# Kernel tuning notes

Hardware: AMD Instinct MI355X
Metric: run time of the kernel (lower is better)

## Reference

```python
import jax, jax.numpy as jnp
import numpy as np

N, C, H, W = 32, 512, 32, 32
K = 64  # num_clusters
D_OUT = 256


def _l2n(v, axis):
    # torch F.normalize: v / max(||v||, 1e-12)
    n = jnp.linalg.norm(v, axis=axis, keepdims=True)
    return v / jnp.maximum(n, 1e-12)


def _bn(v, gamma, beta):
    # BatchNorm1d, training mode (batch stats, biased variance), eps=1e-5
    m = v.mean(axis=0)
    var = ((v - m) ** 2).mean(axis=0)
    return (v - m) / jnp.sqrt(var + 1e-5) * gamma + beta


def setup_inputs() -> dict:
    key = jax.random.key(0)
    ks = jax.random.split(key, 5)
    x = jax.random.normal(ks[0], (N, C, H, W), dtype=jnp.float32)
    conv_w = jax.random.normal(ks[1], (K, C), dtype=jnp.float32) * 0.05
    centroids = jax.random.uniform(ks[2], (K, C), dtype=jnp.float32)
    hidden_w = jax.random.normal(ks[3], (K * C, D_OUT), dtype=jnp.float32) / jnp.sqrt(jnp.float32(C))
    gating_w = jax.random.normal(ks[4], (D_OUT, D_OUT), dtype=jnp.float32) / jnp.sqrt(jnp.float32(D_OUT))
    return {
        "x": x,
        "conv_w": conv_w,
        "centroids": centroids,
        "hidden_w": hidden_w,
        "bn2_gamma": jnp.ones((D_OUT,), jnp.float32),
        "bn2_beta": jnp.zeros((D_OUT,), jnp.float32),
        "gating_w": gating_w,
        "gbn_gamma": jnp.ones((D_OUT,), jnp.float32),
        "gbn_beta": jnp.zeros((D_OUT,), jnp.float32),
    }


def reference(x, conv_w, centroids, hidden_w, bn2_gamma, bn2_beta, gating_w, gbn_gamma, gbn_beta):
    n = x.shape[0]
    # descriptor-wise L2 normalization over channel dim
    x = _l2n(x, axis=1)                                  # [N,C,H,W]
    xf = x.reshape(n, x.shape[1], -1)                    # [N,C,S]
    # 1x1 conv -> soft assignment, softmax over clusters
    sa = jnp.einsum('ncs,kc->nks', xf, conv_w)           # [N,K,S]
    sa = jax.nn.softmax(sa, axis=1)
    # matmul-form NetVLAD: sum_s a[n,k,s]*(x[n,c,s]-cent[k,c])
    vlad = jnp.einsum('nks,ncs->nkc', sa, xf) \
         - sa.sum(axis=-1)[..., None] * centroids[None]  # [N,K,C]
    vlad = _l2n(vlad, axis=2)                            # intra-normalization
    vlad = _l2n(vlad.reshape(n, -1), axis=1)             # [N,K*C]
    v = vlad @ hidden_w                                  # [N,256]
    v = _bn(v, bn2_gamma, bn2_beta)
    # context gating
    gates = jax.nn.sigmoid(_bn(v @ gating_w, gbn_gamma, gbn_beta))
    return v * gates
```

## Files before the change

kernel.cpp:

```cpp
#include <hip/hip_runtime.h>
#include <math.h>

static constexpr int Nb = 32;
static constexpr int Cc = 512;
static constexpr int Ss = 1024;
static constexpr int Kk = 64;
static constexpr int Dd = 256;

typedef __attribute__((ext_vector_type(8))) short bf16x8;
typedef __attribute__((ext_vector_type(4))) float f32x4;
typedef __attribute__((ext_vector_type(4))) unsigned int u32x4;

union FragU { u32x4 u; bf16x8 h; };

__device__ __forceinline__ unsigned hi_pack(float x0, float x1) {
    return __builtin_amdgcn_perm(__float_as_uint(x1), __float_as_uint(x0), 0x07060302u);
}
__device__ __forceinline__ float trunc_hi(float x) {
    return __uint_as_float(__float_as_uint(x) & 0xFFFF0000u);
}
__device__ __forceinline__ void split8(const float* xv, FragU& bh, FragU& bl) {
#pragma unroll
    for (int p = 0; p < 4; ++p) {
        bh.u[p] = hi_pack(xv[2*p], xv[2*p+1]);
        float l0 = xv[2*p]   - trunc_hi(xv[2*p]);
        float l1 = xv[2*p+1] - trunc_hi(xv[2*p+1]);
        bl.u[p] = hi_pack(l0, l1);
    }
}

__device__ __forceinline__ void gload_lds16(const void* g, void* l) {
    __builtin_amdgcn_global_load_lds(
        (const __attribute__((address_space(1))) void*)g,
        (__attribute__((address_space(3))) void*)l, 16, 0, 0);
}

__global__ __launch_bounds__(256) void kprep_cw(
    const float* __restrict__ cw, short* __restrict__ cwh, short* __restrict__ cwl)
{
    int t = blockIdx.x * 256 + threadIdx.x;
    float4 v = *(const float4*)&cw[4 * (size_t)t];
    unsigned h0 = hi_pack(v.x, v.y), h1 = hi_pack(v.z, v.w);
    float l0 = v.x - trunc_hi(v.x), l1 = v.y - trunc_hi(v.y);
    float l2 = v.z - trunc_hi(v.z), l3 = v.w - trunc_hi(v.w);
    unsigned g0 = hi_pack(l0, l1), g1 = hi_pack(l2, l3);
    ((uint2*)cwh)[t] = make_uint2(h0, h1);
    ((uint2*)cwl)[t] = make_uint2(g0, g1);
}

__global__ __launch_bounds__(512) void k1_sa(
    const float* __restrict__ x, const short* __restrict__ cw_hi,
    const short* __restrict__ cw_lo, short* __restrict__ a_hi,
    short* __restrict__ a_lo, float* __restrict__ asum_part)
{
    __shared__ float xt[3 * 2048];
    __shared__ short cwh_t[3 * 4096];
    __shared__ short cwl_t[3 * 4096];
    __shared__ float redm[4][32];
    __shared__ float reds[4][32];

    const int tid = threadIdx.x;
    const int w = tid >> 6, lane = tid & 63;
    const int m = w & 3, sg = w >> 2;
    const int l15 = lane & 15, lg = lane >> 4;
    const int n = blockIdx.y, s0 = blockIdx.x * 32;

    const int strow = lane >> 3;
    const int stchk = lane & 7;
    const int xrow = 8 * w + strow;
    const int krow = 8 * w + strow;
    const int cwchk = stchk ^ (krow & 7);

    const float* xsrc = x + (size_t)n * Cc * Ss + s0 + 4 * stchk;

    auto GL = [&](int t) {
        const int b = t % 3;
        gload_lds16(xsrc + (size_t)(t * 64 + xrow) * Ss,
                    (char*)xt + b * 8192 + w * 1024);
        gload_lds16(cw_hi + (size_t)krow * Cc + t * 64 + cwchk * 8,
                    (char*)cwh_t + b * 8192 + w * 1024);
        gload_lds16(cw_lo + (size_t)krow * Cc + t * 64 + cwchk * 8,
                    (char*)cwl_t + b * 8192 + w * 1024);
    };

    f32x4 acc = {0.f, 0.f, 0.f, 0.f};
    float ssq = 0.f;
    const int sl = 16 * sg + l15;

    GL(0);
    GL(1);

    for (int ct = 0; ct < 8; ++ct) {
        if (ct < 7) { asm volatile("s_waitcnt vmcnt(3)" ::: "memory"); }
        else        { asm volatile("s_waitcnt vmcnt(0)" ::: "memory"); }
        __builtin_amdgcn_sched_barrier(0);
        __builtin_amdgcn_s_barrier();
        __builtin_amdgcn_sched_barrier(0);

        const int b = ct % 3;
#pragma unroll
        for (int ks = 0; ks < 2; ++ks) {
            const int cb = 32 * ks + 8 * lg;
            float xv[8];
#pragma unroll
            for (int j = 0; j < 8; ++j) xv[j] = xt[b * 2048 + (cb + j) * 32 + sl];
#pragma unroll
            for (int j = 0; j < 8; ++j) ssq += xv[j] * xv[j];
            FragU bh, bl;
            split8(xv, bh, bl);
            FragU ah, al;
            const int cslot = ((4 * ks + lg) ^ (l15 & 7)) * 8;
            ah.u = *(const u32x4*)&cwh_t[b * 4096 + (16 * m + l15) * 64 + cslot];
            al.u = *(const u32x4*)&cwl_t[b * 4096 + (16 * m + l15) * 64 + cslot];
            acc = __builtin_amdgcn_mfma_f32_16x16x32_bf16(al.h, bh.h, acc, 0, 0, 0);
            acc = __builtin_amdgcn_mfma_f32_16x16x32_bf16(ah.h, bl.h, acc, 0, 0, 0);
            acc = __builtin_amdgcn_mfma_f32_16x16x32_bf16(ah.h, bh.h, acc, 0, 0, 0);
        }
        if (ct < 6) GL(ct + 2);
    }

    ssq += __shfl_xor(ssq, 16);
    ssq += __shfl_xor(ssq, 32);
    const float inv = 1.f / fmaxf(sqrtf(ssq), 1e-12f);

    float sv[4];
    float mmax = -1e30f;
#pragma unroll
    for (int r = 0; r < 4; ++r) {
        sv[r] = acc[r] * inv;
        mmax = fmaxf(mmax, sv[r]);
    }
    mmax = fmaxf(mmax, __shfl_xor(mmax, 16));
    mmax = fmaxf(mmax, __shfl_xor(mmax, 32));
    if (lg == 0) redm[m][sl] = mmax;
    __syncthreads();
    mmax = fmaxf(fmaxf(redm[0][sl], redm[1][sl]),
                 fmaxf(redm[2][sl], redm[3][sl]));
    float den = 0.f;
#pragma unroll
    for (int r = 0; r < 4; ++r) {
        sv[r] = expf(sv[r] - mmax);
        den += sv[r];
    }
    den += __shfl_xor(den, 16);
    den += __shfl_xor(den, 32);
    if (lg == 0) reds[m][sl] = den;
    __syncthreads();
    den = reds[0][sl] + reds[1][sl] + reds[2][sl] + reds[3][sl];
    const float rinv = 1.f / den;

    const int scol = s0 + sl;
#pragma unroll
    for (int r = 0; r < 4; ++r) {
        const float a = sv[r] * rinv;
        const int k = 16 * m + 4 * lg + r;
        float t = a;
        t += __shfl_xor(t, 1); t += __shfl_xor(t, 2);
        t += __shfl_xor(t, 4); t += __shfl_xor(t, 8);
        if (l15 == 0)
            asum_part[((size_t)(n * Kk + k) << 6) + blockIdx.x * 2 + sg] = t;
        const float av = a * inv;
        const unsigned u = __float_as_uint(av);
        const float hv = __uint_as_float(u & 0xFFFF0000u);
        const size_t idx = (size_t)(n * Kk + k) * Ss + scol;
        a_hi[idx] = (short)(u >> 16);
        a_lo[idx] = (short)(__float_as_uint(av - hv) >> 16);
    }
}

__global__ __launch_bounds__(256) void kasum(
    const float* __restrict__ asum_part, float* __restrict__ asum)
{
    int row = blockIdx.x * 256 + threadIdx.x;
    const float* p = &asum_part[(size_t)row << 6];
    float s = 0.f;
#pragma unroll
    for (int i = 0; i < 16; ++i) {
        float4 v = *(const float4*)&p[4 * i];
        s += v.x + v.y + v.z + v.w;
    }
    asum[row] = s;
}

__global__ __launch_bounds__(512) void k2_vlad(
    const float* __restrict__ x, const short* __restrict__ a_hi,
    const short* __restrict__ a_lo, const float* __restrict__ centroids,
    const float* __restrict__ asum, float* __restrict__ vp0,
    float* __restrict__ vp1)
{
    __shared__ float xt[3 * 2048];
    __shared__ float asum_l[64];

    const int tid = threadIdx.x;
    const int w = tid >> 6, lane = tid & 63;
    const int wq = w & 3, wh = w >> 2;
    const int l15 = lane & 15, lg = lane >> 4;
    const int n = blockIdx.x, cp = blockIdx.y, sh = blockIdx.z;

    if (sh == 1 && tid < 64) asum_l[tid] = asum[n * Kk + tid];

    const int strow = lane >> 3;
    const int xrow = 8 * w + strow;
    const int stchk = (lane & 7) ^ (xrow & 7);
    const float* xsrc = x + (size_t)(n * Cc + cp * 64 + xrow) * Ss
                      + sh * 512 + 4 * stchk;

    auto GLx = [&](int t) {
        gload_lds16(xsrc + t * 32, (char*)xt + (t % 3) * 8192 + w * 1024);
    };

    const short* ahb = a_hi + (size_t)n * Kk * Ss + sh * 512;
    const short* alb = a_lo + (size_t)n * Kk * Ss + sh * 512;
    const int m0 = 2 * wh, m1 = 2 * wh + 1;
    const size_t arow0 = (size_t)(16 * m0 + l15) * Ss;
    const size_t arow1 = (size_t)(16 * m1 + l15) * Ss;

    f32x4 zero4 = {0.f, 0.f, 0.f, 0.f};
    f32x4 acc0 = zero4, acc1 = zero4;

    FragU ah0c, al0c, ah1c, al1c;
    FragU ah0n, al0n, ah1n, al1n;

    GLx(0);
    GLx(1);
    {
        const int so = 8 * lg;
        ah0c.u = *(const u32x4*)&ahb[arow0 + so];
        al0c.u = *(const u32x4*)&alb[arow0 + so];
        ah1c.u = *(const u32x4*)&ahb[arow1 + so];
        al1c.u = *(const u32x4*)&alb[arow1 + so];
    }

    for (int t = 0; t < 16; ++t) {
        if (t < 15) { asm volatile("s_waitcnt vmcnt(5)" ::: "memory"); }
        else        { asm volatile("s_waitcnt vmcnt(4)" ::: "memory"); }
        __builtin_amdgcn_sched_barrier(0);
        __builtin_amdgcn_s_barrier();
        __builtin_amdgcn_sched_barrier(0);

        if (t < 15) {
            const int so = (t + 1) * 32 + 8 * lg;
            ah0n.u = *(const u32x4*)&ahb[arow0 + so];
            al0n.u = *(const u32x4*)&alb[arow0 + so];
            ah1n.u = *(const u32x4*)&ahb[arow1 + so];
            al1n.u = *(const u32x4*)&alb[arow1 + so];
        }

        const int b = t % 3;
        const int cl = 16 * wq + l15;
        const int q0 = (2 * lg)     ^ (l15 & 7);
        const int q1 = (2 * lg + 1) ^ (l15 & 7);
        float4 xq0 = *(const float4*)&xt[b * 2048 + cl * 32 + q0 * 4];
        float4 xq1 = *(const float4*)&xt[b * 2048 + cl * 32 + q1 * 4];
        float xv[8] = {xq0.x, xq0.y, xq0.z, xq0.w, xq1.x, xq1.y, xq1.z, xq1.w};
        FragU bh, bl;
        split8(xv, bh, bl);

        acc0 = __builtin_amdgcn_mfma_f32_16x16x32_bf16(al0c.h, bh.h, acc0, 0, 0, 0);
        acc0 = __builtin_amdgcn_mfma_f32_16x16x32_bf16(ah0c.h, bl.h, acc0, 0, 0, 0);
        acc0 = __builtin_amdgcn_mfma_f32_16x16x32_bf16(ah0c.h, bh.h, acc0, 0, 0, 0);
        acc1 = __builtin_amdgcn_mfma_f32_16x16x32_bf16(al1c.h, bh.h, acc1, 0, 0, 0);
        acc1 = __builtin_amdgcn_mfma_f32_16x16x32_bf16(ah1c.h, bl.h, acc1, 0, 0, 0);
        acc1 = __builtin_amdgcn_mfma_f32_16x16x32_bf16(ah1c.h, bh.h, acc1, 0, 0, 0);

        ah0c.u = ah0n.u; al0c.u = al0n.u;
        ah1c.u = ah1n.u; al1c.u = al1n.u;

        if (t < 14) GLx(t + 2);
    }

    float* dst = sh ? vp1 : vp0;
    const int c = cp * 64 + 16 * wq + l15;
#pragma unroll
    for (int mi = 0; mi < 2; ++mi) {
        const f32x4 a4 = mi ? acc1 : acc0;
        const int m = 2 * wh + mi;
#pragma unroll
        for (int r = 0; r < 4; ++r) {
            const int k = 16 * m + 4 * lg + r;
            float val = a4[r];
            if (sh == 1) val -= asum_l[k] * centroids[(size_t)k * Cc + c];
            dst[(size_t)(n * Kk + k) * Cc + c] = val;
        }
    }
}

__global__ __launch_bounds__(512) void k3a_norm(
    float* __restrict__ vlad, const float* __restrict__ vp1,
    float* __restrict__ nrm)
{
    const int tid = threadIdx.x;
    const int w = tid >> 6, lane = tid & 63;
    const int n = blockIdx.x, kg = blockIdx.y;
    const int row = (n * Kk) + kg * 8 + w;
    const size_t base = (size_t)row * Cc + lane * 8;

    float4 v0 = *(const float4*)&vlad[base];
    float4 v1 = *(const float4*)&vlad[base + 4];
    float4 u0 = *(const float4*)&vp1[base];
    float4 u1 = *(const float4*)&vp1[base + 4];
    v0.x += u0.x; v0.y += u0.y; v0.z += u0.z; v0.w += u0.w;
    v1.x += u1.x; v1.y += u1.y; v1.z += u1.z; v1.w += u1.w;
    *(float4*)&vlad[base] = v0;
    *(float4*)&vlad[base + 4] = v1;
    float ssq = v0.x*v0.x + v0.y*v0.y + v0.z*v0.z + v0.w*v0.w
              + v1.x*v1.x + v1.y*v1.y + v1.z*v1.z + v1.w*v1.w;
#pragma unroll
    for (int off = 32; off >= 1; off >>= 1) ssq += __shfl_xor(ssq, off);
    if (lane == 0) nrm[row] = sqrtf(ssq);
}

__global__ __launch_bounds__(64) void k3b_scale(
    const float* __restrict__ nrm, float* __restrict__ scale)
{
    const int n = blockIdx.x, k = threadIdx.x;
    float r = nrm[n * Kk + k];
    float rn = r / fmaxf(r, 1e-12f);
    float p = rn * rn;
#pragma unroll
    for (int off = 32; off >= 1; off >>= 1) p += __shfl_xor(p, off);
    float g = sqrtf(p);
    scale[n * Kk + k] = 1.f / (fmaxf(r, 1e-12f) * fmaxf(g, 1e-12f));
}

__global__ __launch_bounds__(512) void k4_hidden(
    const float* __restrict__ vlad, const float* __restrict__ scale,
    const float* __restrict__ hw, float* __restrict__ vpart)
{
    __shared__ float vl[128][33];
    __shared__ float scale_l[32];
    const int tid = threadIdx.x;
    const int kc0 = blockIdx.x * 128;
    const int k = kc0 >> 9;
    if (tid < 32) scale_l[tid] = scale[tid * Kk + k];
    __syncthreads();
#pragma unroll
    for (int i = 0; i < 8; ++i) {
        int idx = tid + i * 512;
        int nn = idx >> 7, kcl = idx & 127;
        vl[kcl][nn] = vlad[(size_t)nn * (Kk * Cc) + kc0 + kcl] * scale_l[nn];
    }
    __syncthreads();

    const int d4 = tid & 63, ng = tid >> 6;
    float4 acc4[4];
#pragma unroll
    for (int j = 0; j < 4; ++j) acc4[j] = make_float4(0.f, 0.f, 0.f, 0.f);

    for (int kcl = 0; kcl < 128; ++kcl) {
        const float4 wv = *(const float4*)&hw[(size_t)(kc0 + kcl) * Dd + d4 * 4];
#pragma unroll
        for (int j = 0; j < 4; ++j) {
            float vn = vl[kcl][4 * ng + j];
            acc4[j].x += vn * wv.x; acc4[j].y += vn * wv.y;
            acc4[j].z += vn * wv.z; acc4[j].w += vn * wv.w;
        }
    }
#pragma unroll
    for (int j = 0; j < 4; ++j)
        *(float4*)&vpart[((size_t)blockIdx.x * Nb + 4 * ng + j) * Dd + d4 * 4] = acc4[j];
}

__global__ __launch_bounds__(128) void k5a_reduce(
    const float* __restrict__ vpart, float* __restrict__ v)
{
    int flat = blockIdx.x * 128 + threadIdx.x;
    float s = 0.f;
#pragma unroll 8
    for (int ch = 0; ch < 256; ++ch) s += vpart[(size_t)ch * (Nb * Dd) + flat];
    v[flat] = s;
}

__global__ __launch_bounds__(256) void k5bc_gate(
    const float* __restrict__ v, const float* __restrict__ gamma,
    const float* __restrict__ beta, const float* __restrict__ gw,
    float* __restrict__ v_bn, float* __restrict__ g_raw)
{
    __shared__ float vb[Dd];
    const int n = blockIdx.x, d = threadIdx.x;

    float s1 = 0.f;
#pragma unroll 8
    for (int i = 0; i < Nb; ++i) s1 += v[i * Dd + d];
    float mean = s1 * (1.f / Nb);
    float var = 0.f;
#pragma unroll 8
    for (int i = 0; i < Nb; ++i) {
        float t = v[i * Dd + d] - mean;
        var += t * t;
    }
    var *= (1.f / Nb);
    float inv = rsqrtf(var + 1e-5f);
    float vbn = (v[n * Dd + d] - mean) * inv * gamma[d] + beta[d];
    vb[d] = vbn;
    v_bn[n * Dd + d] = vbn;
    __syncthreads();

    float acc = 0.f;
#pragma unroll 8
    for (int c = 0; c < Dd; ++c) acc += vb[c] * gw[c * Dd + d];
    g_raw[n * Dd + d] = acc;
}

__global__ __launch_bounds__(256) void k5d_out(
    const float* __restrict__ g_raw, const float* __restrict__ v_bn,
    const float* __restrict__ ggamma, const float* __restrict__ gbeta,
    float* __restrict__ out)
{
    const int d = threadIdx.x;
    float vals[Nb];
    float s1 = 0.f;
#pragma unroll
    for (int n = 0; n < Nb; ++n) {
        vals[n] = g_raw[n * Dd + d];
        s1 += vals[n];
    }
    float m = s1 * (1.f / Nb);
    float var = 0.f;
#pragma unroll
    for (int n = 0; n < Nb; ++n) {
        float t = vals[n] - m;
        var += t * t;
    }
    var *= (1.f / Nb);
    float inv = rsqrtf(var + 1e-5f);
    float g = ggamma[d], b = gbeta[d];
#pragma unroll
    for (int n = 0; n < Nb; ++n) {
        float t = (vals[n] - m) * inv * g + b;
        float sg = 1.f / (1.f + expf(-t));
        out[n * Dd + d] = v_bn[n * Dd + d] * sg;
    }
}

extern "C" void kernel_launch(void* const* d_in, const int* in_sizes, int n_in,
                              void* d_out, int out_size, void* d_ws, size_t ws_size,
                              hipStream_t stream)
{
    const float* x         = (const float*)d_in[0];
    const float* conv_w    = (const float*)d_in[1];
    const float* centroids = (const float*)d_in[2];
    const float* hidden_w  = (const float*)d_in[3];
    const float* bn2_gamma = (const float*)d_in[4];
    const float* bn2_beta  = (const float*)d_in[5];
    const float* gating_w  = (const float*)d_in[6];
    const float* gbn_gamma = (const float*)d_in[7];
    const float* gbn_beta  = (const float*)d_in[8];
    float* out = (float*)d_out;

    char* B = (char*)d_ws;
    short* a_hi      = (short*)(B);
    short* a_lo      = (short*)(B + (4u << 20));
    float* vp0       = (float*)(B + (8u << 20));
    float* vp1       = (float*)(B + (12u << 20));
    short* cw_hi     = (short*)(B + (16u << 20));
    short* cw_lo     = (short*)(B + (16u << 20) + 65536u);
    float* asum_part = (float*)(B + (16u << 20) + 131072u);
    float* asum      = (float*)(B + (16u << 20) + 655360u);
    float* nrm       = asum + 2048;
    float* scale     = nrm + 2048;
    float* v         = scale + 2048;
    float* v_bn      = v + 8192;
    float* g_raw     = v_bn + 8192;
    float* vpart     = (float*)B;

    kprep_cw<<<32, 256, 0, stream>>>(conv_w, cw_hi, cw_lo);
    k1_sa<<<dim3(32, 32), 512, 0, stream>>>(x, cw_hi, cw_lo, a_hi, a_lo, asum_part);
    kasum<<<8, 256, 0, stream>>>(asum_part, asum);
    k2_vlad<<<dim3(32, 8, 2), 512, 0, stream>>>(x, a_hi, a_lo, centroids, asum, vp0, vp1);
    k3a_norm<<<dim3(32, 8), 512, 0, stream>>>(vp0, vp1, nrm);
    k3b_scale<<<32, 64, 0, stream>>>(nrm, scale);
    k4_hidden<<<256, 512, 0, stream>>>(vp0, scale, hidden_w, vpart);
    k5a_reduce<<<64, 128, 0, stream>>>(vpart, v);
    k5bc_gate<<<32, 256, 0, stream>>>(v, bn2_gamma, bn2_beta, gating_w, v_bn, g_raw);
    k5d_out<<<1, 256, 0, stream>>>(g_raw, v_bn, gbn_gamma, gbn_beta, out);
}
```

Before: 117.2 us.

## Drop split-S in vlad kernel and fuse asum, partial-sum merge, and norm

The vlad kernel no longer splits the spatial dimension across two blocks. Each block now loops over all 1024 positions, which removes the vp1 partial buffer and the k3a_norm pass that added the two halves. The asum reduction and the per-row squared-norm partials are folded into the vlad kernel, cutting the kasum and k3a launches and the extra global round trips. In exchange the vlad grid drops from 512 to 256 blocks and each block runs a loop twice as long, which lowers parallelism on a GPU with many CUs.

New measurement: 116.7 us. About the same (-0.5%).

```diff
diff --git a/kernel.cpp b/kernel.cpp
--- a/kernel.cpp
+++ b/kernel.cpp
@@ -168,49 +168,44 @@
     }
 }
 
-__global__ __launch_bounds__(256) void kasum(
-    const float* __restrict__ asum_part, float* __restrict__ asum)
-{
-    int row = blockIdx.x * 256 + threadIdx.x;
-    const float* p = &asum_part[(size_t)row << 6];
-    float s = 0.f;
-#pragma unroll
-    for (int i = 0; i < 16; ++i) {
-        float4 v = *(const float4*)&p[4 * i];
-        s += v.x + v.y + v.z + v.w;
-    }
-    asum[row] = s;
-}
-
 __global__ __launch_bounds__(512) void k2_vlad(
     const float* __restrict__ x, const short* __restrict__ a_hi,
     const short* __restrict__ a_lo, const float* __restrict__ centroids,
-    const float* __restrict__ asum, float* __restrict__ vp0,
-    float* __restrict__ vp1)
+    const float* __restrict__ asum_part, float* __restrict__ vlad,
+    float* __restrict__ nrm_part)
 {
     __shared__ float xt[3 * 2048];
     __shared__ float asum_l[64];
+    __shared__ float nssq[4][64];
 
     const int tid = threadIdx.x;
     const int w = tid >> 6, lane = tid & 63;
     const int wq = w & 3, wh = w >> 2;
     const int l15 = lane & 15, lg = lane >> 4;
-    const int n = blockIdx.x, cp = blockIdx.y, sh = blockIdx.z;
-
-    if (sh == 1 && tid < 64) asum_l[tid] = asum[n * Kk + tid];
+    const int n = blockIdx.x, cp = blockIdx.y;
+
+    if (tid < 64) {
+        const float* p = &asum_part[(size_t)(n * Kk + tid) << 6];
+        float s = 0.f;
+#pragma unroll
+        for (int i = 0; i < 16; ++i) {
+            float4 q = *(const float4*)&p[4 * i];
+            s += q.x + q.y + q.z + q.w;
+        }
+        asum_l[tid] = s;
+    }
 
     const int strow = lane >> 3;
     const int xrow = 8 * w + strow;
     const int stchk = (lane & 7) ^ (xrow & 7);
-    const float* xsrc = x + (size_t)(n * Cc + cp * 64 + xrow) * Ss
-                      + sh * 512 + 4 * stchk;
+    const float* xsrc = x + (size_t)(n * Cc + cp * 64 + xrow) * Ss + 4 * stchk;
 
     auto GLx = [&](int t) {
         gload_lds16(xsrc + t * 32, (char*)xt + (t % 3) * 8192 + w * 1024);
     };
 
-    const short* ahb = a_hi + (size_t)n * Kk * Ss + sh * 512;
-    const short* alb = a_lo + (size_t)n * Kk * Ss + sh * 512;
+    const short* ahb = a_hi + (size_t)n * Kk * Ss;
+    const short* alb = a_lo + (size_t)n * Kk * Ss;
     const int m0 = 2 * wh, m1 = 2 * wh + 1;
     const size_t arow0 = (size_t)(16 * m0 + l15) * Ss;
     const size_t arow1 = (size_t)(16 * m1 + l15) * Ss;
@@ -231,14 +226,14 @@
         al1c.u = *(const u32x4*)&alb[arow1 + so];
     }
 
-    for (int t = 0; t < 16; ++t) {
-        if (t < 15) { asm volatile("s_waitcnt vmcnt(5)" ::: "memory"); }
+    for (int t = 0; t < 32; ++t) {
+        if (t < 31) { asm volatile("s_waitcnt vmcnt(5)" ::: "memory"); }
         else        { asm volatile("s_waitcnt vmcnt(4)" ::: "memory"); }
         __builtin_amdgcn_sched_barrier(0);
         __builtin_amdgcn_s_barrier();
         __builtin_amdgcn_sched_barrier(0);
 
-        if (t < 15) {
+        if (t < 31) {
             const int so = (t + 1) * 32 + 8 * lg;
             ah0n.u = *(const u32x4*)&ahb[arow0 + so];
             al0n.u = *(const u32x4*)&alb[arow0 + so];
@@ -266,10 +261,9 @@
         ah0c.u = ah0n.u; al0c.u = al0n.u;
         ah1c.u = ah1n.u; al1c.u = al1n.u;
 
-        if (t < 14) GLx(t + 2);
-    }
-
-    float* dst = sh ? vp1 : vp0;
+        if (t < 30) GLx(t + 2);
+    }
+
     const int c = cp * 64 + 16 * wq + l15;
 #pragma unroll
     for (int mi = 0; mi < 2; ++mi) {
@@ -278,48 +272,35 @@
 #pragma unroll
         for (int r = 0; r < 4; ++r) {
             const int k = 16 * m + 4 * lg + r;
-            float val = a4[r];
-            if (sh == 1) val -= asum_l[k] * centroids[(size_t)k * Cc + c];
-            dst[(size_t)(n * Kk + k) * Cc + c] = val;
+            float val = a4[r] - asum_l[k] * centroids[(size_t)k * Cc + c];
+            vlad[(size_t)(n * Kk + k) * Cc + c] = val;
+            float ss = val * val;
+            ss += __shfl_xor(ss, 1); ss += __shfl_xor(ss, 2);
+            ss += __shfl_xor(ss, 4); ss += __shfl_xor(ss, 8);
+            if (l15 == 0) nssq[wq][k] = ss;
         }
     }
-}
-
-__global__ __launch_bounds__(512) void k3a_norm(
-    float* __restrict__ vlad, const float* __restrict__ vp1,
-    float* __restrict__ nrm)
-{
-    const int tid = threadIdx.x;
-    const int w = tid >> 6, lane = tid & 63;
-    const int n = blockIdx.x, kg = blockIdx.y;
-    const int row = (n * Kk) + kg * 8 + w;
-    const size_t base = (size_t)row * Cc + lane * 8;
-
-    float4 v0 = *(const float4*)&vlad[base];
-    float4 v1 = *(const float4*)&vlad[base + 4];
-    float4 u0 = *(const float4*)&vp1[base];
-    float4 u1 = *(const float4*)&vp1[base + 4];
-    v0.x += u0.x; v0.y += u0.y; v0.z += u0.z; v0.w += u0.w;
-    v1.x += u1.x; v1.y += u1.y; v1.z += u1.z; v1.w += u1.w;
-    *(float4*)&vlad[base] = v0;
-    *(float4*)&vlad[base + 4] = v1;
-    float ssq = v0.x*v0.x + v0.y*v0.y + v0.z*v0.z + v0.w*v0.w
-              + v1.x*v1.x + v1.y*v1.y + v1.z*v1.z + v1.w*v1.w;
-#pragma unroll
-    for (int off = 32; off >= 1; off >>= 1) ssq += __shfl_xor(ssq, off);
-    if (lane == 0) nrm[row] = sqrtf(ssq);
-}
-
-__global__ __launch_bounds__(64) void k3b_scale(
-    const float* __restrict__ nrm, float* __restrict__ scale)
+    __syncthreads();
+    if (tid < 64) {
+        float s = nssq[0][tid] + nssq[1][tid] + nssq[2][tid] + nssq[3][tid];
+        nrm_part[((size_t)(n * Kk + tid) << 3) + cp] = s;
+    }
+}
+
+__global__ __launch_bounds__(64) void k3s_scale(
+    const float* __restrict__ nrm_part, float* __restrict__ scale)
 {
     const int n = blockIdx.x, k = threadIdx.x;
-    float r = nrm[n * Kk + k];
+    const float* p = &nrm_part[(size_t)(n * Kk + k) << 3];
+    float ssq = 0.f;
+#pragma unroll
+    for (int i = 0; i < 8; ++i) ssq += p[i];
+    float r = sqrtf(ssq);
     float rn = r / fmaxf(r, 1e-12f);
-    float p = rn * rn;
-#pragma unroll
-    for (int off = 32; off >= 1; off >>= 1) p += __shfl_xor(p, off);
-    float g = sqrtf(p);
+    float pw = rn * rn;
+#pragma unroll
+    for (int off = 32; off >= 1; off >>= 1) pw += __shfl_xor(pw, off);
+    float g = sqrtf(pw);
     scale[n * Kk + k] = 1.f / (fmaxf(r, 1e-12f) * fmaxf(g, 1e-12f));
 }
 
@@ -451,14 +432,12 @@
     char* B = (char*)d_ws;
     short* a_hi      = (short*)(B);
     short* a_lo      = (short*)(B + (4u << 20));
-    float* vp0       = (float*)(B + (8u << 20));
-    float* vp1       = (float*)(B + (12u << 20));
-    short* cw_hi     = (short*)(B + (16u << 20));
-    short* cw_lo     = (short*)(B + (16u << 20) + 65536u);
-    float* asum_part = (float*)(B + (16u << 20) + 131072u);
-    float* asum      = (float*)(B + (16u << 20) + 655360u);
-    float* nrm       = asum + 2048;
-    float* scale     = nrm + 2048;
+    float* vlad      = (float*)(B + (8u << 20));
+    short* cw_hi     = (short*)(B + (12u << 20));
+    short* cw_lo     = (short*)(B + (12u << 20) + 65536u);
+    float* asum_part = (float*)(B + (12u << 20) + 131072u);
+    float* nrm_part  = (float*)(B + (12u << 20) + 655360u);
+    float* scale     = (float*)(B + (12u << 20) + 720896u);
     float* v         = scale + 2048;
     float* v_bn      = v + 8192;
     float* g_raw     = v_bn + 8192;
@@ -466,11 +445,9 @@
 
     kprep_cw<<<32, 256, 0, stream>>>(conv_w, cw_hi, cw_lo);
     k1_sa<<<dim3(32, 32), 512, 0, stream>>>(x, cw_hi, cw_lo, a_hi, a_lo, asum_part);
-    kasum<<<8, 256, 0, stream>>>(asum_part, asum);
-    k2_vlad<<<dim3(32, 8, 2), 512, 0, stream>>>(x, a_hi, a_lo, centroids, asum, vp0, vp1);
-    k3a_norm<<<dim3(32, 8), 512, 0, stream>>>(vp0, vp1, nrm);
-    k3b_scale<<<32, 64, 0, stream>>>(nrm, scale);
-    k4_hidden<<<256, 512, 0, stream>>>(vp0, scale, hidden_w, vpart);
+    k2_vlad<<<dim3(32, 8), 512, 0, stream>>>(x, a_hi, a_lo, centroids, asum_part, vlad, nrm_part);
+    k3s_scale<<<32, 64, 0, stream>>>(nrm_part, scale);
+    k4_hidden<<<256, 512, 0, stream>>>(vlad, scale, hidden_w, vpart);
     k5a_reduce<<<64, 128, 0, stream>>>(vpart, v);
     k5bc_gate<<<32, 256, 0, stream>>>(v, bn2_gamma, bn2_beta, gating_w, v_bn, g_raw);
     k5d_out<<<1, 256, 0, stream>>>(g_raw, v_bn, gbn_gamma, gbn_beta, out);
```
